# Kernel tuning notes

Measured on AMD Instinct MI355X. Metric: run time of the kernel, lower is better.

The kernel has to match this reference:

```python
import math
import jax, jax.numpy as jnp
import numpy as np

B, T, D, H = 4, 2048, 256, 4
DK = D // H
P = 2 * T - 1  # relative position length


def setup_inputs() -> dict:
    key = jax.random.key(0)
    ks = jax.random.split(key, 16)
    s = 0.02
    inp = {
        "query": jax.random.normal(ks[0], (B, T, D), jnp.float32),
        "key": jax.random.normal(ks[1], (B, T, D), jnp.float32),
        "value": jax.random.normal(ks[2], (B, T, D), jnp.float32),
        "pos_emb": jax.random.normal(ks[3], (1, P, D), jnp.float32),
        "mask": jnp.ones((B, 1, T), jnp.int32),
        "Wq": jax.random.normal(ks[4], (D, D), jnp.float32) * s,
        "bq": jnp.zeros((D,), jnp.float32),
        "Wk": jax.random.normal(ks[5], (D, D), jnp.float32) * s,
        "bk": jnp.zeros((D,), jnp.float32),
        "Wv": jax.random.normal(ks[6], (D, D), jnp.float32) * s,
        "bv": jnp.zeros((D,), jnp.float32),
        "Wpos": jax.random.normal(ks[7], (D, D), jnp.float32) * s,
        "pos_bias_u": jax.random.normal(ks[8], (H, DK), jnp.float32) * s,
        "pos_bias_v": jax.random.normal(ks[9], (H, DK), jnp.float32) * s,
        "Wo": jax.random.normal(ks[10], (D, D), jnp.float32) * s,
        "bo": jnp.zeros((D,), jnp.float32),
    }
    return inp


def rel_shift(x):
    # x: (B, H, T, P) with P = 2T-1  ->  (B, H, T, T)
    b, h, t, p = x.shape
    x_pad = jnp.pad(x, ((0, 0), (0, 0), (0, 0), (1, 0)))  # (B,H,T,P+1)
    x_pad = x_pad.reshape(b, h, p + 1, t)
    x = x_pad[:, :, 1:].reshape(b, h, t, p)
    return x[..., : p // 2 + 1]


def reference(query, key, value, pos_emb, mask, Wq, bq, Wk, bk, Wv, bv,
              Wpos, pos_bias_u, pos_bias_v, Wo, bo):
    b = query.shape[0]
    q = (query @ Wq.T + bq).reshape(b, -1, H, DK)              # (B,T,H,DK)
    k = (key @ Wk.T + bk).reshape(b, -1, H, DK).transpose(0, 2, 1, 3)    # (B,H,T,DK)
    v = (value @ Wv.T + bv).reshape(b, -1, H, DK).transpose(0, 2, 1, 3)  # (B,H,T,DK)
    p = (pos_emb @ Wpos.T).reshape(pos_emb.shape[0], -1, H, DK).transpose(0, 2, 1, 3)  # (1,H,P,DK)

    q_u = (q + pos_bias_u).transpose(0, 2, 1, 3)  # (B,H,T,DK)
    q_v = (q + pos_bias_v).transpose(0, 2, 1, 3)

    matrix_ac = jnp.matmul(q_u, k.transpose(0, 1, 3, 2))  # (B,H,T,T)
    matrix_bd = jnp.matmul(q_v, p.transpose(0, 1, 3, 2))  # (B,H,T,P), batch broadcast
    matrix_bd = rel_shift(matrix_bd)                       # (B,H,T,T)

    scores = (matrix_ac + matrix_bd) / math.sqrt(DK)
    m = (mask[:, None] == 0)  # (B,1,1,T) bool
    scores = jnp.where(m, jnp.float32(-1e9), scores)
    attn = jax.nn.softmax(scores, axis=-1)
    attn = jnp.where(m, jnp.float32(0.0), attn)

    x = jnp.matmul(attn, v)                               # (B,H,T,DK)
    x = x.transpose(0, 2, 1, 3).reshape(b, -1, H * DK)    # (B,T,D)
    return x @ Wo.T + bo
```

## Files before the change

kernel.cpp:

```cpp
#include <hip/hip_runtime.h>
#include <hip/hip_bf16.h>
#include <string.h>

#define Bc 4
#define Tc 2048
#define Dc 256
#define Hc 4
#define DKc 64
#define Pc 4095

typedef short bf16x8 __attribute__((ext_vector_type(8)));
typedef float f32x4 __attribute__((ext_vector_type(4)));

__device__ __forceinline__ unsigned short f2bs(float x) {
    __bf16 b = (__bf16)x;
    return __builtin_bit_cast(unsigned short, b);
}
__device__ __forceinline__ float bs2f(unsigned short u) {
    unsigned int x = ((unsigned int)u) << 16;
    return __builtin_bit_cast(float, x);
}

__device__ __forceinline__ void gemm_body(
    const float* __restrict__ A, const float* __restrict__ Wt,
    const float* __restrict__ bias, const float* __restrict__ addv,
    unsigned short* __restrict__ outp, int M, int Tdim, float scale,
    unsigned short* sa, unsigned short* sb)
{
    const int tid = threadIdx.x;
    const int wv = tid >> 6, lane = tid & 63;
    const int c = lane & 15, g = lane >> 4;
    const int m0 = blockIdx.x * 64, n0 = blockIdx.y * 64;
    const int tb = wv * 16;

    f32x4 acc[4];
    #pragma unroll
    for (int ct = 0; ct < 4; ct++) acc[ct] = (f32x4){0.f, 0.f, 0.f, 0.f};

    for (int k0 = 0; k0 < 256; k0 += 64) {
        if (k0) __syncthreads();
        #pragma unroll
        for (int r = 0; r < 2; r++) {
            int lin = tid + 256 * r;
            int row = lin >> 3, ch = lin & 7;
            int gm = m0 + row;
            float4 f0, f1;
            if (gm < M) {
                f0 = *(const float4*)(A + (size_t)gm * 256 + k0 + ch * 8);
                f1 = *(const float4*)(A + (size_t)gm * 256 + k0 + ch * 8 + 4);
            } else {
                f0 = make_float4(0.f, 0.f, 0.f, 0.f); f1 = f0;
            }
            unsigned short pa[8] = {f2bs(f0.x), f2bs(f0.y), f2bs(f0.z), f2bs(f0.w),
                                    f2bs(f1.x), f2bs(f1.y), f2bs(f1.z), f2bs(f1.w)};
            *(uint4*)&sa[row * 72 + ch * 8] = *(const uint4*)pa;

            float4 w0 = *(const float4*)(Wt + (size_t)(n0 + row) * 256 + k0 + ch * 8);
            float4 w1 = *(const float4*)(Wt + (size_t)(n0 + row) * 256 + k0 + ch * 8 + 4);
            unsigned short pb[8] = {f2bs(w0.x), f2bs(w0.y), f2bs(w0.z), f2bs(w0.w),
                                    f2bs(w1.x), f2bs(w1.y), f2bs(w1.z), f2bs(w1.w)};
            *(uint4*)&sb[row * 72 + ch * 8] = *(const uint4*)pb;
        }
        __syncthreads();
        #pragma unroll
        for (int kk = 0; kk < 2; kk++) {
            bf16x8 af = *(const bf16x8*)&sa[(tb + c) * 72 + kk * 32 + g * 8];
            #pragma unroll
            for (int ct = 0; ct < 4; ct++) {
                bf16x8 bf = *(const bf16x8*)&sb[(ct * 16 + c) * 72 + kk * 32 + g * 8];
                acc[ct] = __builtin_amdgcn_mfma_f32_16x16x32_bf16(af, bf, acc[ct], 0, 0, 0);
            }
        }
    }

    __syncthreads();
    #pragma unroll
    for (int ct = 0; ct < 4; ct++) {
        int n = n0 + ct * 16 + c;
        float badd = (bias ? bias[n] : 0.f) + (addv ? addv[n] : 0.f);
        #pragma unroll
        for (int r = 0; r < 4; r++)
            sa[(tb + g * 4 + r) * 72 + ct * 16 + c] = f2bs((acc[ct][r] + badd) * scale);
    }
    __syncthreads();
    const int hh = n0 >> 6;
    #pragma unroll
    for (int r = 0; r < 2; r++) {
        int lin = tid + 256 * r;
        int row = lin >> 3, ch = lin & 7;
        int gm = m0 + row;
        if (gm >= M) continue;
        int bb = gm / Tdim, t = gm - bb * Tdim;
        size_t oidx = ((size_t)(bb * Hc + hh) * Tdim + t) * DKc + ch * 8;
        *(uint4*)&outp[oidx] = *(const uint4*)&sa[row * 72 + ch * 8];
    }
}

__global__ __launch_bounds__(256) void gemm_qkv(
    const float* __restrict__ q, const float* __restrict__ k, const float* __restrict__ v,
    const float* __restrict__ Wq, const float* __restrict__ bq,
    const float* __restrict__ Wk, const float* __restrict__ bk,
    const float* __restrict__ Wv, const float* __restrict__ bv,
    const float* __restrict__ pbu,
    unsigned short* __restrict__ qo, unsigned short* __restrict__ ko,
    unsigned short* __restrict__ vo)
{
    __shared__ unsigned short sa[64 * 72];
    __shared__ unsigned short sb[64 * 72];
    const float *A, *Wt, *bias, *addv; unsigned short* outp; float scale;
    if (blockIdx.z == 0)      { A = q; Wt = Wq; bias = bq; addv = pbu;    outp = qo; scale = 0.125f; }
    else if (blockIdx.z == 1) { A = k; Wt = Wk; bias = bk; addv = nullptr; outp = ko; scale = 1.f; }
    else                      { A = v; Wt = Wv; bias = bv; addv = nullptr; outp = vo; scale = 1.f; }
    gemm_body(A, Wt, bias, addv, outp, Bc * Tc, Tc, scale, sa, sb);
}

__global__ __launch_bounds__(256) void gemm_p(
    const float* __restrict__ pos_emb, const float* __restrict__ Wpos,
    const float* __restrict__ pbu, const float* __restrict__ pbv,
    unsigned short* __restrict__ ph_b, float* __restrict__ dpw)
{
    __shared__ unsigned short sa[64 * 72];
    __shared__ unsigned short sb[64 * 72];
    gemm_body(pos_emb, Wpos, nullptr, nullptr, ph_b, Pc, Pc, 1.f, sa, sb);
    const int tid = threadIdx.x;
    const int m0 = blockIdx.x * 64, h = blockIdx.y;
    if (tid < 64) {
        int w = m0 + tid;
        if (w < Pc) {
            float acc = 0.f;
            #pragma unroll
            for (int dk = 0; dk < DKc; dk++)
                acc = fmaf(pbv[h * DKc + dk] - pbu[h * DKc + dk],
                           bs2f(sa[tid * 72 + dk]), acc);
            dpw[h * Pc + w] = acc * 0.125f;
        }
    }
}

__global__ __launch_bounds__(256) void gemm_out_split(
    const unsigned short* __restrict__ Ahi,
    const unsigned short* __restrict__ Alo,
    const float* __restrict__ Wo,
    const float* __restrict__ bias,
    float* __restrict__ outp, int M)
{
    __shared__ unsigned short sah[64 * 72];
    __shared__ unsigned short sal[64 * 72];
    __shared__ unsigned short sbh[64 * 72];
    __shared__ unsigned short sbl[64 * 72];
    __shared__ float sout[64 * 68];
    const int tid = threadIdx.x;
    const int wv = tid >> 6, lane = tid & 63;
    const int c = lane & 15, g = lane >> 4;
    const int m0 = blockIdx.x * 64, n0 = blockIdx.y * 64;
    const int tb = wv * 16;

    f32x4 acc[4];
    #pragma unroll
    for (int ct = 0; ct < 4; ct++) acc[ct] = (f32x4){0.f, 0.f, 0.f, 0.f};

    for (int k0 = 0; k0 < 256; k0 += 64) {
        if (k0) __syncthreads();
        #pragma unroll
        for (int r = 0; r < 2; r++) {
            int lin = tid + 256 * r;
            int row = lin >> 3, ch = lin & 7;
            size_t asrc = (size_t)(m0 + row) * 256 + k0 + ch * 8;
            *(uint4*)&sah[row * 72 + ch * 8] = *(const uint4*)(Ahi + asrc);
            *(uint4*)&sal[row * 72 + ch * 8] = *(const uint4*)(Alo + asrc);
            float4 w0 = *(const float4*)(Wo + (size_t)(n0 + row) * 256 + k0 + ch * 8);
            float4 w1 = *(const float4*)(Wo + (size_t)(n0 + row) * 256 + k0 + ch * 8 + 4);
            float we[8] = {w0.x, w0.y, w0.z, w0.w, w1.x, w1.y, w1.z, w1.w};
            unsigned short phi[8], plo[8];
            #pragma unroll
            for (int e = 0; e < 8; e++) {
                unsigned short hi = f2bs(we[e]);
                phi[e] = hi;
                plo[e] = f2bs(we[e] - bs2f(hi));
            }
            *(uint4*)&sbh[row * 72 + ch * 8] = *(const uint4*)phi;
            *(uint4*)&sbl[row * 72 + ch * 8] = *(const uint4*)plo;
        }
        __syncthreads();
        #pragma unroll
        for (int kk = 0; kk < 2; kk++) {
            bf16x8 ah = *(const bf16x8*)&sah[(tb + c) * 72 + kk * 32 + g * 8];
            bf16x8 al = *(const bf16x8*)&sal[(tb + c) * 72 + kk * 32 + g * 8];
            #pragma unroll
            for (int ct = 0; ct < 4; ct++) {
                bf16x8 bh = *(const bf16x8*)&sbh[(ct * 16 + c) * 72 + kk * 32 + g * 8];
                bf16x8 bl = *(const bf16x8*)&sbl[(ct * 16 + c) * 72 + kk * 32 + g * 8];
                acc[ct] = __builtin_amdgcn_mfma_f32_16x16x32_bf16(ah, bh, acc[ct], 0, 0, 0);
                acc[ct] = __builtin_amdgcn_mfma_f32_16x16x32_bf16(ah, bl, acc[ct], 0, 0, 0);
                acc[ct] = __builtin_amdgcn_mfma_f32_16x16x32_bf16(al, bh, acc[ct], 0, 0, 0);
            }
        }
    }

    __syncthreads();
    #pragma unroll
    for (int ct = 0; ct < 4; ct++) {
        float b = bias[n0 + ct * 16 + c];
        #pragma unroll
        for (int r = 0; r < 4; r++)
            sout[(tb + g * 4 + r) * 68 + ct * 16 + c] = acc[ct][r] + b;
    }
    __syncthreads();
    #pragma unroll
    for (int r = 0; r < 4; r++) {
        int lin = tid + 256 * r;
        int row = lin >> 4, c4 = lin & 15;
        float4 v = *(const float4*)&sout[row * 68 + c4 * 4];
        *(float4*)&outp[(size_t)(m0 + row) * 256 + n0 + c4 * 4] = v;
    }
}

__global__ __launch_bounds__(512) void attn_mfma(
    const unsigned short* __restrict__ qu,
    const unsigned short* __restrict__ kh,
    const unsigned short* __restrict__ vh,
    const unsigned short* __restrict__ ph,
    const float* __restrict__ dpw_g,
    const int*   __restrict__ mask,
    unsigned short* __restrict__ xhi,
    unsigned short* __restrict__ xlo)
{
    __shared__ unsigned short sq[128 * 72];
    __shared__ unsigned short sk[64 * 72];
    __shared__ unsigned short svt[64 * 72];
    __shared__ unsigned short sp[128 * 72];
    __shared__ unsigned short spw[256 * 72];
    __shared__ float sbdw[8][16 * 84];
    __shared__ float sdpw[256];
    __shared__ float smask[64];

    const int tid = threadIdx.x;
    const int wv = tid >> 6;
    const int lane = tid & 63;
    const int c = lane & 15, g = lane >> 4;
    const int bh = blockIdx.x, b = bh >> 2, h = bh & 3;
    const int t0 = blockIdx.y * 128;
    const int tb = wv * 16;
    const int base0 = Tc - 128 - t0;

    const unsigned short* qbase = qu + ((size_t)bh * Tc + t0) * DKc;
    const unsigned short* kbase = kh + (size_t)bh * Tc * DKc;
    const unsigned short* vbase = vh + (size_t)bh * Tc * DKc;
    const unsigned short* pbase = ph + (size_t)h * Pc * DKc;

    const int srow = tid >> 3, sch = tid & 7;

    #pragma unroll
    for (int r = 0; r < 2; r++) {
        int lin = tid + 512 * r;
        int row = lin >> 3, ch = lin & 7;
        *(uint4*)&sq[row * 72 + ch * 8] =
            *(const uint4*)(qbase + (size_t)row * DKc + ch * 8);
        int a0 = base0 + row;
        *(uint4*)&spw[(a0 & 255) * 72 + ch * 8] =
            *(const uint4*)(pbase + (size_t)a0 * DKc + ch * 8);
    }
    if (tid < 128) sdpw[(base0 + tid) & 255] = dpw_g[h * Pc + base0 + tid];

    f32x4 O[4];
    #pragma unroll
    for (int ct = 0; ct < 4; ct++) O[ct] = (f32x4){0.f, 0.f, 0.f, 0.f};
    float mrow[4], lrow[4];
    #pragma unroll
    for (int r = 0; r < 4; r++) { mrow[r] = -3.0e38f; lrow[r] = 0.f; }

    bf16x8 qf0, qf1;

    for (int kt = 0; kt < Tc / 64; kt++) {
        const int j0 = kt * 64;
        const int relb = base0 + kt * 64;
        __syncthreads();

        *(uint4*)&sk[srow * 72 + sch * 8] =
            *(const uint4*)(kbase + (size_t)(j0 + srow) * DKc + sch * 8);
        {
            uint4 raw = *(const uint4*)(vbase + (size_t)(j0 + srow) * DKc + sch * 8);
            unsigned short el[8];
            __builtin_memcpy(el, &raw, 16);
            #pragma unroll
            for (int e = 0; e < 8; e++) {
                int dk = sch * 8 + e;
                svt[dk * 72 + (srow ^ ((dk >> 3) << 3))] = el[e];
            }
        }
        {
            int pabs = relb + 128 + srow;
            int psrc = pabs <= Pc - 1 ? pabs : Pc - 1;
            *(uint4*)&spw[(pabs & 255) * 72 + sch * 8] =
                *(const uint4*)(pbase + (size_t)psrc * DKc + sch * 8);
        }
        if (tid < 64) {
            int da = relb + 128 + tid;
            sdpw[da & 255] = dpw_g[h * Pc + (da <= Pc - 1 ? da : Pc - 1)];
            smask[tid] = (mask[b * Tc + j0 + tid] == 0) ? -1e9f : 0.f;
        }
        __syncthreads();

        if (kt == 0) {
            qf0 = *(const bf16x8*)&sq[(tb + c) * 72 + g * 8];
            qf1 = *(const bf16x8*)&sq[(tb + c) * 72 + (4 + g) * 8];
        }

        __builtin_amdgcn_s_setprio(1);
        f32x4 sac[4];
        #pragma unroll
        for (int ct = 0; ct < 4; ct++) {
            f32x4 acc = (f32x4){0.f, 0.f, 0.f, 0.f};
            bf16x8 kf0 = *(const bf16x8*)&sk[(ct * 16 + c) * 72 + g * 8];
            bf16x8 kf1 = *(const bf16x8*)&sk[(ct * 16 + c) * 72 + (4 + g) * 8];
            acc = __builtin_amdgcn_mfma_f32_16x16x32_bf16(qf0, kf0, acc, 0, 0, 0);
            acc = __builtin_amdgcn_mfma_f32_16x16x32_bf16(qf1, kf1, acc, 0, 0, 0);
            sac[ct] = acc;
        }

        const int wstart = 112 - tb;
        #pragma unroll
        for (int wt = 0; wt < 5; wt++) {
            f32x4 acc = (f32x4){0.f, 0.f, 0.f, 0.f};
            int plog = wstart + wt * 16 + c;
            int phys = (relb + plog) & 255;
            bf16x8 pf0 = *(const bf16x8*)&spw[phys * 72 + g * 8];
            bf16x8 pf1 = *(const bf16x8*)&spw[phys * 72 + (4 + g) * 8];
            acc = __builtin_amdgcn_mfma_f32_16x16x32_bf16(qf0, pf0, acc, 0, 0, 0);
            acc = __builtin_amdgcn_mfma_f32_16x16x32_bf16(qf1, pf1, acc, 0, 0, 0);
            float dpwv = sdpw[phys];
            #pragma unroll
            for (int r = 0; r < 4; r++)
                sbdw[wv][(g * 4 + r) * 84 + wt * 16 + c] = acc[r] + dpwv;
        }
        __builtin_amdgcn_s_setprio(0);

        float sreg[4][4];
        #pragma unroll
        for (int ct = 0; ct < 4; ct++) {
            float madd = smask[ct * 16 + c];
            #pragma unroll
            for (int r = 0; r < 4; r++) {
                int tt = g * 4 + r;
                int x = ct * 16 + c - tt + 15;
                sreg[ct][r] = sac[ct][r] + sbdw[wv][tt * 84 + x] + madd;
            }
        }

        float tmax[4], tsum[4];
        #pragma unroll
        for (int r = 0; r < 4; r++)
            tmax[r] = fmaxf(fmaxf(sreg[0][r], sreg[1][r]), fmaxf(sreg[2][r], sreg[3][r]));
        #pragma unroll
        for (int off = 1; off < 16; off <<= 1)
            #pragma unroll
            for (int r = 0; r < 4; r++)
                tmax[r] = fmaxf(tmax[r], __shfl_xor(tmax[r], off));

        float mnew[4], scl[4];
        #pragma unroll
        for (int r = 0; r < 4; r++) {
            mnew[r] = fmaxf(mrow[r], tmax[r]);
            scl[r] = __expf(mrow[r] - mnew[r]);
        }
        float pr[4][4];
        #pragma unroll
        for (int r = 0; r < 4; r++) {
            #pragma unroll
            for (int ct = 0; ct < 4; ct++)
                pr[ct][r] = __expf(sreg[ct][r] - mnew[r]);
            tsum[r] = (pr[0][r] + pr[1][r]) + (pr[2][r] + pr[3][r]);
        }
        #pragma unroll
        for (int off = 1; off < 16; off <<= 1)
            #pragma unroll
            for (int r = 0; r < 4; r++)
                tsum[r] += __shfl_xor(tsum[r], off);
        #pragma unroll
        for (int r = 0; r < 4; r++) {
            lrow[r] = lrow[r] * scl[r] + tsum[r];
            mrow[r] = mnew[r];
        }
        #pragma unroll
        for (int ct = 0; ct < 4; ct++) {
            f32x4 o = O[ct];
            o[0] *= scl[0]; o[1] *= scl[1]; o[2] *= scl[2]; o[3] *= scl[3];
            O[ct] = o;
        }

        #pragma unroll
        for (int ct = 0; ct < 4; ct++)
            #pragma unroll
            for (int r = 0; r < 4; r++)
                sp[(tb + g * 4 + r) * 72 + ct * 16 + c] = f2bs(pr[ct][r]);

        __builtin_amdgcn_s_setprio(1);
        #pragma unroll
        for (int js = 0; js < 2; js++) {
            bf16x8 pfrag = *(const bf16x8*)&sp[(tb + c) * 72 + (js * 4 + g) * 8];
            #pragma unroll
            for (int ct = 0; ct < 4; ct++) {
                int dk = ct * 16 + c;
                int tcol = (js * 32 + g * 8) ^ ((dk >> 3) << 3);
                bf16x8 vf = *(const bf16x8*)&svt[dk * 72 + tcol];
                O[ct] = __builtin_amdgcn_mfma_f32_16x16x32_bf16(pfrag, vf, O[ct], 0, 0, 0);
            }
        }
        __builtin_amdgcn_s_setprio(0);
    }

    float invl[4];
    #pragma unroll
    for (int r = 0; r < 4; r++)
        invl[r] = (lrow[r] > 0.f) ? 1.f / lrow[r] : 0.f;
    #pragma unroll
    for (int ct = 0; ct < 4; ct++)
        #pragma unroll
        for (int r = 0; r < 4; r++) {
            size_t idx = ((size_t)(b * Tc + t0 + tb + g * 4 + r)) * Dc + h * DKc + ct * 16 + c;
            float v = O[ct][r] * invl[r];
            unsigned short hi = f2bs(v);
            xhi[idx] = hi;
            xlo[idx] = f2bs(v - bs2f(hi));
        }
}

extern "C" void kernel_launch(void* const* d_in, const int* in_sizes, int n_in,
                              void* d_out, int out_size, void* d_ws, size_t ws_size,
                              hipStream_t stream) {
    const float* query   = (const float*)d_in[0];
    const float* key_    = (const float*)d_in[1];
    const float* value   = (const float*)d_in[2];
    const float* pos_emb = (const float*)d_in[3];
    const int*   mask    = (const int*)d_in[4];
    const float* Wq  = (const float*)d_in[5];
    const float* bq  = (const float*)d_in[6];
    const float* Wk  = (const float*)d_in[7];
    const float* bk  = (const float*)d_in[8];
    const float* Wv  = (const float*)d_in[9];
    const float* bv  = (const float*)d_in[10];
    const float* Wpos = (const float*)d_in[11];
    const float* pbu = (const float*)d_in[12];
    const float* pbv = (const float*)d_in[13];
    const float* Wo  = (const float*)d_in[14];
    const float* bo  = (const float*)d_in[15];
    float* out = (float*)d_out;

    const size_t NQ = (size_t)Bc * Hc * Tc * DKc;
    unsigned short* qu_b = (unsigned short*)d_ws;
    unsigned short* kh_b = qu_b + NQ;
    unsigned short* vh_b = kh_b + NQ;
    unsigned short* ph_b = vh_b + NQ;
    unsigned short* xhi  = ph_b + 1048576;
    unsigned short* xlo  = xhi + NQ;
    float* dpw = (float*)(xlo + NQ);

    gemm_qkv<<<dim3(128, 4, 3), dim3(256), 0, stream>>>(query, key_, value,
        Wq, bq, Wk, bk, Wv, bv, pbu, qu_b, kh_b, vh_b);
    gemm_p<<<dim3(64, 4), dim3(256), 0, stream>>>(pos_emb, Wpos, pbu, pbv, ph_b, dpw);
    attn_mfma<<<dim3(Bc * Hc, Tc / 128), dim3(512), 0, stream>>>(
        qu_b, kh_b, vh_b, ph_b, dpw, mask, xhi, xlo);
    gemm_out_split<<<dim3(128, 4), dim3(256), 0, stream>>>(xhi, xlo, Wo, bo, out, Bc * Tc);
}
```

Before: 223.8 us.

## Register-prefetch next K/V/pos tiles to overlap global loads with MFMA compute

Restructures the attention main loop so the K, V, positional tile, dpw and mask values for tile kt+2 are loaded into registers while tile kt is computed. After compute they are stored into shared memory for the next iteration. The prologue preloads the first tile into shared memory and the second into registers. This hides global-load latency behind MFMA work but adds register pressure at 512 threads per block.

```diff
diff --git a/kernel.cpp b/kernel.cpp
--- a/kernel.cpp
+++ b/kernel.cpp
@@ -214,6 +214,8 @@
         *(float4*)&outp[(size_t)(m0 + row) * 256 + n0 + c4 * 4] = v;
     }
 }
+
+#define NTILES (Tc / 64)
 
 __global__ __launch_bounds__(512) void attn_mfma(
     const unsigned short* __restrict__ qu,
@@ -256,11 +258,43 @@
         int row = lin >> 3, ch = lin & 7;
         *(uint4*)&sq[row * 72 + ch * 8] =
             *(const uint4*)(qbase + (size_t)row * DKc + ch * 8);
+    }
+    #pragma unroll
+    for (int r = 0; r < 3; r++) {
+        int lin = tid + 512 * r;
+        int row = lin >> 3, ch = lin & 7;
         int a0 = base0 + row;
         *(uint4*)&spw[(a0 & 255) * 72 + ch * 8] =
             *(const uint4*)(pbase + (size_t)a0 * DKc + ch * 8);
     }
-    if (tid < 128) sdpw[(base0 + tid) & 255] = dpw_g[h * Pc + base0 + tid];
+    if (tid < 192) sdpw[(base0 + tid) & 255] = dpw_g[h * Pc + base0 + tid];
+    *(uint4*)&sk[srow * 72 + sch * 8] =
+        *(const uint4*)(kbase + (size_t)srow * DKc + sch * 8);
+    {
+        uint4 raw = *(const uint4*)(vbase + (size_t)srow * DKc + sch * 8);
+        unsigned short el[8];
+        __builtin_memcpy(el, &raw, 16);
+        #pragma unroll
+        for (int e = 0; e < 8; e++) {
+            int dk = sch * 8 + e;
+            svt[dk * 72 + (srow ^ ((dk >> 3) << 3))] = el[e];
+        }
+    }
+    if (tid < 64) smask[tid] = (mask[b * Tc + tid] == 0) ? -1e9f : 0.f;
+    __syncthreads();
+
+    uint4 kreg, vreg, preg;
+    float dpwreg = 0.f; int mreg = 1;
+    {
+        kreg = *(const uint4*)(kbase + (size_t)(64 + srow) * DKc + sch * 8);
+        vreg = *(const uint4*)(vbase + (size_t)(64 + srow) * DKc + sch * 8);
+        int pabs = base0 + 64 + 128 + srow;
+        preg = *(const uint4*)(pbase + (size_t)pabs * DKc + sch * 8);
+        if (tid < 64) {
+            dpwreg = dpw_g[h * Pc + pabs - srow + tid];
+            mreg = mask[b * Tc + 64 + tid];
+        }
+    }
 
     f32x4 O[4];
     #pragma unroll
@@ -270,41 +304,11 @@
     for (int r = 0; r < 4; r++) { mrow[r] = -3.0e38f; lrow[r] = 0.f; }
 
     bf16x8 qf0, qf1;
-
-    for (int kt = 0; kt < Tc / 64; kt++) {
-        const int j0 = kt * 64;
+    qf0 = *(const bf16x8*)&sq[(tb + c) * 72 + g * 8];
+    qf1 = *(const bf16x8*)&sq[(tb + c) * 72 + (4 + g) * 8];
+
+    for (int kt = 0; kt < NTILES; kt++) {
         const int relb = base0 + kt * 64;
-        __syncthreads();
-
-        *(uint4*)&sk[srow * 72 + sch * 8] =
-            *(const uint4*)(kbase + (size_t)(j0 + srow) * DKc + sch * 8);
-        {
-            uint4 raw = *(const uint4*)(vbase + (size_t)(j0 + srow) * DKc + sch * 8);
-            unsigned short el[8];
-            __builtin_memcpy(el, &raw, 16);
-            #pragma unroll
-            for (int e = 0; e < 8; e++) {
-                int dk = sch * 8 + e;
-                svt[dk * 72 + (srow ^ ((dk >> 3) << 3))] = el[e];
-            }
-        }
-        {
-            int pabs = relb + 128 + srow;
-            int psrc = pabs <= Pc - 1 ? pabs : Pc - 1;
-            *(uint4*)&spw[(pabs & 255) * 72 + sch * 8] =
-                *(const uint4*)(pbase + (size_t)psrc * DKc + sch * 8);
-        }
-        if (tid < 64) {
-            int da = relb + 128 + tid;
-            sdpw[da & 255] = dpw_g[h * Pc + (da <= Pc - 1 ? da : Pc - 1)];
-            smask[tid] = (mask[b * Tc + j0 + tid] == 0) ? -1e9f : 0.f;
-        }
-        __syncthreads();
-
-        if (kt == 0) {
-            qf0 = *(const bf16x8*)&sq[(tb + c) * 72 + g * 8];
-            qf1 = *(const bf16x8*)&sq[(tb + c) * 72 + (4 + g) * 8];
-        }
 
         __builtin_amdgcn_s_setprio(1);
         f32x4 sac[4];
@@ -407,6 +411,44 @@
             }
         }
         __builtin_amdgcn_s_setprio(0);
+
+        if (kt == NTILES - 1) break;
+
+        __syncthreads();
+        *(uint4*)&sk[srow * 72 + sch * 8] = kreg;
+        {
+            unsigned short el[8];
+            __builtin_memcpy(el, &vreg, 16);
+            #pragma unroll
+            for (int e = 0; e < 8; e++) {
+                int dk = sch * 8 + e;
+                svt[dk * 72 + (srow ^ ((dk >> 3) << 3))] = el[e];
+            }
+        }
+        {
+            int pabs = relb + 64 + 128 + srow;
+            *(uint4*)&spw[(pabs & 255) * 72 + sch * 8] = preg;
+        }
+        if (tid < 64) {
+            int da = relb + 64 + 128 + tid;
+            sdpw[da & 255] = dpwreg;
+            smask[tid] = (mreg == 0) ? -1e9f : 0.f;
+        }
+        __syncthreads();
+
+        if (kt + 2 < NTILES) {
+            const int j0n = (kt + 2) * 64;
+            kreg = *(const uint4*)(kbase + (size_t)(j0n + srow) * DKc + sch * 8);
+            vreg = *(const uint4*)(vbase + (size_t)(j0n + srow) * DKc + sch * 8);
+            int pabs = base0 + j0n + 128 + srow;
+            int psrc = pabs <= Pc - 1 ? pabs : Pc - 1;
+            preg = *(const uint4*)(pbase + (size_t)psrc * DKc + sch * 8);
+            if (tid < 64) {
+                int da = base0 + j0n + 128 + tid;
+                dpwreg = dpw_g[h * Pc + (da <= Pc - 1 ? da : Pc - 1)];
+                mreg = mask[b * Tc + j0n + tid];
+            }
+        }
     }
 
     float invl[4];
```

After: 211.5 us. 1.06x faster.

## Pre-transpose V in projection, prefetch K/V tiles, shuffle-based rel-shift

Applied to the files above, without the earlier changes.

The V projection now writes V already transposed (DK x T), so the attention kernel can load it into shared memory with plain vector stores instead of a per-element scatter. K, V and the mask for the next tile are prefetched into registers one tile ahead. Q fragments are loaded straight from global memory, and the positional tiles are read directly from global or cache, which removes the spw/sbdw/sdpw/sq shared buffers and lowers LDS use. The relative shift is rebuilt with cross-lane shuffles instead of a shared-memory round trip. The cost is more global loads of P rows per tile and extra shuffle instructions.

```diff
diff --git a/kernel.cpp b/kernel.cpp
--- a/kernel.cpp
+++ b/kernel.cpp
@@ -1,6 +1,5 @@
 #include <hip/hip_runtime.h>
 #include <hip/hip_bf16.h>
-#include <string.h>
 
 #define Bc 4
 #define Tc 2048
@@ -25,7 +24,7 @@
     const float* __restrict__ A, const float* __restrict__ Wt,
     const float* __restrict__ bias, const float* __restrict__ addv,
     unsigned short* __restrict__ outp, int M, int Tdim, float scale,
-    unsigned short* sa, unsigned short* sb)
+    int outmode, unsigned short* sa, unsigned short* sb)
 {
     const int tid = threadIdx.x;
     const int wv = tid >> 6, lane = tid & 63;
@@ -74,25 +73,41 @@
     }
 
     __syncthreads();
+    const int ld = (outmode == 3) ? 66 : 72;
     #pragma unroll
     for (int ct = 0; ct < 4; ct++) {
         int n = n0 + ct * 16 + c;
         float badd = (bias ? bias[n] : 0.f) + (addv ? addv[n] : 0.f);
         #pragma unroll
         for (int r = 0; r < 4; r++)
-            sa[(tb + g * 4 + r) * 72 + ct * 16 + c] = f2bs((acc[ct][r] + badd) * scale);
+            sa[(tb + g * 4 + r) * ld + ct * 16 + c] = f2bs((acc[ct][r] + badd) * scale);
     }
     __syncthreads();
     const int hh = n0 >> 6;
-    #pragma unroll
-    for (int r = 0; r < 2; r++) {
-        int lin = tid + 256 * r;
-        int row = lin >> 3, ch = lin & 7;
-        int gm = m0 + row;
-        if (gm >= M) continue;
-        int bb = gm / Tdim, t = gm - bb * Tdim;
-        size_t oidx = ((size_t)(bb * Hc + hh) * Tdim + t) * DKc + ch * 8;
-        *(uint4*)&outp[oidx] = *(const uint4*)&sa[row * 72 + ch * 8];
+    if (outmode == 3) {
+        const int bb = m0 / Tdim, trow0 = m0 - (m0 / Tdim) * Tdim;
+        #pragma unroll
+        for (int r = 0; r < 2; r++) {
+            int lin = tid + 256 * r;
+            int dk = lin >> 3, tch = lin & 7;
+            unsigned short tmp[8];
+            #pragma unroll
+            for (int e = 0; e < 8; e++)
+                tmp[e] = sa[(tch * 8 + e) * 66 + dk];
+            size_t oidx = ((size_t)(bb * Hc + hh) * DKc + dk) * Tdim + trow0 + tch * 8;
+            *(uint4*)&outp[oidx] = *(const uint4*)tmp;
+        }
+    } else {
+        #pragma unroll
+        for (int r = 0; r < 2; r++) {
+            int lin = tid + 256 * r;
+            int row = lin >> 3, ch = lin & 7;
+            int gm = m0 + row;
+            if (gm >= M) continue;
+            int bb = gm / Tdim, t = gm - bb * Tdim;
+            size_t oidx = ((size_t)(bb * Hc + hh) * Tdim + t) * DKc + ch * 8;
+            *(uint4*)&outp[oidx] = *(const uint4*)&sa[row * 72 + ch * 8];
+        }
     }
 }
 
@@ -107,11 +122,11 @@
 {
     __shared__ unsigned short sa[64 * 72];
     __shared__ unsigned short sb[64 * 72];
-    const float *A, *Wt, *bias, *addv; unsigned short* outp; float scale;
-    if (blockIdx.z == 0)      { A = q; Wt = Wq; bias = bq; addv = pbu;    outp = qo; scale = 0.125f; }
-    else if (blockIdx.z == 1) { A = k; Wt = Wk; bias = bk; addv = nullptr; outp = ko; scale = 1.f; }
-    else                      { A = v; Wt = Wv; bias = bv; addv = nullptr; outp = vo; scale = 1.f; }
-    gemm_body(A, Wt, bias, addv, outp, Bc * Tc, Tc, scale, sa, sb);
+    const float *A, *Wt, *bias, *addv; unsigned short* outp; float scale; int mode;
+    if (blockIdx.z == 0)      { A = q; Wt = Wq; bias = bq; addv = pbu;     outp = qo; scale = 0.125f; mode = 2; }
+    else if (blockIdx.z == 1) { A = k; Wt = Wk; bias = bk; addv = nullptr; outp = ko; scale = 1.f;    mode = 2; }
+    else                      { A = v; Wt = Wv; bias = bv; addv = nullptr; outp = vo; scale = 1.f;    mode = 3; }
+    gemm_body(A, Wt, bias, addv, outp, Bc * Tc, Tc, scale, mode, sa, sb);
 }
 
 __global__ __launch_bounds__(256) void gemm_p(
@@ -121,7 +136,7 @@
 {
     __shared__ unsigned short sa[64 * 72];
     __shared__ unsigned short sb[64 * 72];
-    gemm_body(pos_emb, Wpos, nullptr, nullptr, ph_b, Pc, Pc, 1.f, sa, sb);
+    gemm_body(pos_emb, Wpos, nullptr, nullptr, ph_b, Pc, Pc, 1.f, 2, sa, sb);
     const int tid = threadIdx.x;
     const int m0 = blockIdx.x * 64, h = blockIdx.y;
     if (tid < 64) {
@@ -215,23 +230,21 @@
     }
 }
 
+#define NTILES (Tc / 64)
+
 __global__ __launch_bounds__(512) void attn_mfma(
     const unsigned short* __restrict__ qu,
     const unsigned short* __restrict__ kh,
-    const unsigned short* __restrict__ vh,
+    const unsigned short* __restrict__ vt,
     const unsigned short* __restrict__ ph,
     const float* __restrict__ dpw_g,
     const int*   __restrict__ mask,
     unsigned short* __restrict__ xhi,
     unsigned short* __restrict__ xlo)
 {
-    __shared__ unsigned short sq[128 * 72];
     __shared__ unsigned short sk[64 * 72];
     __shared__ unsigned short svt[64 * 72];
     __shared__ unsigned short sp[128 * 72];
-    __shared__ unsigned short spw[256 * 72];
-    __shared__ float sbdw[8][16 * 84];
-    __shared__ float sdpw[256];
     __shared__ float smask[64];
 
     const int tid = threadIdx.x;
@@ -245,22 +258,26 @@
 
     const unsigned short* qbase = qu + ((size_t)bh * Tc + t0) * DKc;
     const unsigned short* kbase = kh + (size_t)bh * Tc * DKc;
-    const unsigned short* vbase = vh + (size_t)bh * Tc * DKc;
+    const unsigned short* vtbase = vt + (size_t)bh * DKc * Tc;
     const unsigned short* pbase = ph + (size_t)h * Pc * DKc;
+    const float* dpwbase = dpw_g + h * Pc;
 
     const int srow = tid >> 3, sch = tid & 7;
 
-    #pragma unroll
-    for (int r = 0; r < 2; r++) {
-        int lin = tid + 512 * r;
-        int row = lin >> 3, ch = lin & 7;
-        *(uint4*)&sq[row * 72 + ch * 8] =
-            *(const uint4*)(qbase + (size_t)row * DKc + ch * 8);
-        int a0 = base0 + row;
-        *(uint4*)&spw[(a0 & 255) * 72 + ch * 8] =
-            *(const uint4*)(pbase + (size_t)a0 * DKc + ch * 8);
-    }
-    if (tid < 128) sdpw[(base0 + tid) & 255] = dpw_g[h * Pc + base0 + tid];
+    bf16x8 qf0 = *(const bf16x8*)(qbase + (size_t)(tb + c) * DKc + g * 8);
+    bf16x8 qf1 = *(const bf16x8*)(qbase + (size_t)(tb + c) * DKc + 32 + g * 8);
+
+    *(uint4*)&sk[srow * 72 + sch * 8] =
+        *(const uint4*)(kbase + (size_t)srow * DKc + sch * 8);
+    *(uint4*)&svt[srow * 72 + ((sch * 8) ^ ((srow >> 3) << 3))] =
+        *(const uint4*)(vtbase + (size_t)srow * Tc + sch * 8);
+    if (tid < 64) smask[tid] = (mask[b * Tc + tid] == 0) ? -1e9f : 0.f;
+    __syncthreads();
+
+    uint4 kreg, vreg; int mreg = 1;
+    kreg = *(const uint4*)(kbase + (size_t)(64 + srow) * DKc + sch * 8);
+    vreg = *(const uint4*)(vtbase + (size_t)srow * Tc + 64 + sch * 8);
+    if (tid < 64) mreg = mask[b * Tc + 64 + tid];
 
     f32x4 O[4];
     #pragma unroll
@@ -269,42 +286,8 @@
     #pragma unroll
     for (int r = 0; r < 4; r++) { mrow[r] = -3.0e38f; lrow[r] = 0.f; }
 
-    bf16x8 qf0, qf1;
-
-    for (int kt = 0; kt < Tc / 64; kt++) {
-        const int j0 = kt * 64;
+    for (int kt = 0; kt < NTILES; kt++) {
         const int relb = base0 + kt * 64;
-        __syncthreads();
-
-        *(uint4*)&sk[srow * 72 + sch * 8] =
-            *(const uint4*)(kbase + (size_t)(j0 + srow) * DKc + sch * 8);
-        {
-            uint4 raw = *(const uint4*)(vbase + (size_t)(j0 + srow) * DKc + sch * 8);
-            unsigned short el[8];
-            __builtin_memcpy(el, &raw, 16);
-            #pragma unroll
-            for (int e = 0; e < 8; e++) {
-                int dk = sch * 8 + e;
-                svt[dk * 72 + (srow ^ ((dk >> 3) << 3))] = el[e];
-            }
-        }
-        {
-            int pabs = relb + 128 + srow;
-            int psrc = pabs <= Pc - 1 ? pabs : Pc - 1;
-            *(uint4*)&spw[(pabs & 255) * 72 + sch * 8] =
-                *(const uint4*)(pbase + (size_t)psrc * DKc + sch * 8);
-        }
-        if (tid < 64) {
-            int da = relb + 128 + tid;
-            sdpw[da & 255] = dpw_g[h * Pc + (da <= Pc - 1 ? da : Pc - 1)];
-            smask[tid] = (mask[b * Tc + j0 + tid] == 0) ? -1e9f : 0.f;
-        }
-        __syncthreads();
-
-        if (kt == 0) {
-            qf0 = *(const bf16x8*)&sq[(tb + c) * 72 + g * 8];
-            qf1 = *(const bf16x8*)&sq[(tb + c) * 72 + (4 + g) * 8];
-        }
 
         __builtin_amdgcn_s_setprio(1);
         f32x4 sac[4];
@@ -319,32 +302,44 @@
         }
 
         const int wstart = 112 - tb;
+        f32x4 accB[5];
         #pragma unroll
         for (int wt = 0; wt < 5; wt++) {
-            f32x4 acc = (f32x4){0.f, 0.f, 0.f, 0.f};
-            int plog = wstart + wt * 16 + c;
-            int phys = (relb + plog) & 255;
-            bf16x8 pf0 = *(const bf16x8*)&spw[phys * 72 + g * 8];
-            bf16x8 pf1 = *(const bf16x8*)&spw[phys * 72 + (4 + g) * 8];
-            acc = __builtin_amdgcn_mfma_f32_16x16x32_bf16(qf0, pf0, acc, 0, 0, 0);
-            acc = __builtin_amdgcn_mfma_f32_16x16x32_bf16(qf1, pf1, acc, 0, 0, 0);
-            float dpwv = sdpw[phys];
-            #pragma unroll
-            for (int r = 0; r < 4; r++)
-                sbdw[wv][(g * 4 + r) * 84 + wt * 16 + c] = acc[r] + dpwv;
+            int pabs = relb + wstart + wt * 16 + c;
+            if (pabs > Pc - 1) pabs = Pc - 1;
+            const unsigned short* prow = pbase + (size_t)pabs * DKc;
+            bf16x8 pf0 = *(const bf16x8*)(prow + g * 8);
+            bf16x8 pf1 = *(const bf16x8*)(prow + 32 + g * 8);
+            f32x4 a = (f32x4){0.f, 0.f, 0.f, 0.f};
+            a = __builtin_amdgcn_mfma_f32_16x16x32_bf16(qf0, pf0, a, 0, 0, 0);
+            a = __builtin_amdgcn_mfma_f32_16x16x32_bf16(qf1, pf1, a, 0, 0, 0);
+            float dpwv = dpwbase[pabs];
+            a[0] += dpwv; a[1] += dpwv; a[2] += dpwv; a[3] += dpwv;
+            accB[wt] = a;
         }
         __builtin_amdgcn_s_setprio(0);
 
         float sreg[4][4];
+        #pragma unroll
+        for (int r = 0; r < 4; r++) {
+            int idx = c - 4 * g - r + 15;
+            int src = 16 * g + (idx & 15);
+            bool hi = (idx >> 4) != 0;
+            float b0 = __shfl(accB[0][r], src);
+            float b1 = __shfl(accB[1][r], src);
+            float b2 = __shfl(accB[2][r], src);
+            float b3 = __shfl(accB[3][r], src);
+            float b4 = __shfl(accB[4][r], src);
+            sreg[0][r] = sac[0][r] + (hi ? b1 : b0);
+            sreg[1][r] = sac[1][r] + (hi ? b2 : b1);
+            sreg[2][r] = sac[2][r] + (hi ? b3 : b2);
+            sreg[3][r] = sac[3][r] + (hi ? b4 : b3);
+        }
         #pragma unroll
         for (int ct = 0; ct < 4; ct++) {
             float madd = smask[ct * 16 + c];
             #pragma unroll
-            for (int r = 0; r < 4; r++) {
-                int tt = g * 4 + r;
-                int x = ct * 16 + c - tt + 15;
-                sreg[ct][r] = sac[ct][r] + sbdw[wv][tt * 84 + x] + madd;
-            }
+            for (int r = 0; r < 4; r++) sreg[ct][r] += madd;
         }
 
         float tmax[4], tsum[4];
@@ -407,6 +402,21 @@
             }
         }
         __builtin_amdgcn_s_setprio(0);
+
+        if (kt == NTILES - 1) break;
+
+        __syncthreads();
+        *(uint4*)&sk[srow * 72 + sch * 8] = kreg;
+        *(uint4*)&svt[srow * 72 + ((sch * 8) ^ ((srow >> 3) << 3))] = vreg;
+        if (tid < 64) smask[tid] = (mreg == 0) ? -1e9f : 0.f;
+        __syncthreads();
+
+        if (kt + 2 < NTILES) {
+            const int j0n = (kt + 2) * 64;
+            kreg = *(const uint4*)(kbase + (size_t)(j0n + srow) * DKc + sch * 8);
+            vreg = *(const uint4*)(vtbase + (size_t)srow * Tc + j0n + sch * 8);
+            if (tid < 64) mreg = mask[b * Tc + j0n + tid];
+        }
     }
 
     float invl[4];
@@ -449,16 +459,16 @@
     const size_t NQ = (size_t)Bc * Hc * Tc * DKc;
     unsigned short* qu_b = (unsigned short*)d_ws;
     unsigned short* kh_b = qu_b + NQ;
-    unsigned short* vh_b = kh_b + NQ;
-    unsigned short* ph_b = vh_b + NQ;
+    unsigned short* vt_b = kh_b + NQ;
+    unsigned short* ph_b = vt_b + NQ;
     unsigned short* xhi  = ph_b + 1048576;
     unsigned short* xlo  = xhi + NQ;
     float* dpw = (float*)(xlo + NQ);
 
     gemm_qkv<<<dim3(128, 4, 3), dim3(256), 0, stream>>>(query, key_, value,
-        Wq, bq, Wk, bk, Wv, bv, pbu, qu_b, kh_b, vh_b);
+        Wq, bq, Wk, bk, Wv, bv, pbu, qu_b, kh_b, vt_b);
     gemm_p<<<dim3(64, 4), dim3(256), 0, stream>>>(pos_emb, Wpos, pbu, pbv, ph_b, dpw);
     attn_mfma<<<dim3(Bc * Hc, Tc / 128), dim3(512), 0, stream>>>(
-        qu_b, kh_b, vh_b, ph_b, dpw, mask, xhi, xlo);
+        qu_b, kh_b, vt_b, ph_b, dpw, mask, xhi, xlo);
     gemm_out_split<<<dim3(128, 4), dim3(256), 0, stream>>>(xhi, xlo, Wo, bo, out, Bc * Tc);
 }
```

After: 295.2 us. 31.9% more time.
